# Kernel optimization log

Hardware: AMD Instinct MI355X
Metric: run time of the kernel (lower is better)

Reference implementation:

```python
import jax, jax.numpy as jnp
import numpy as np

NX = 1024
N_HEAD = 16
HEAD_DIM = NX // N_HEAD
RPE_MAX = 20
LN_EPS = 1e-5


def _layernorm(h, g, b, eps=LN_EPS):
    mu = jnp.mean(h, axis=-1, keepdims=True)
    var = jnp.var(h, axis=-1, keepdims=True)
    return (h - mu) * jax.lax.rsqrt(var + eps) * g + b


def setup_inputs() -> dict:
    key = jax.random.key(0)
    ks = jax.random.split(key, 12)
    B, S = 2, 1024
    x = jax.random.normal(ks[0], (B, S, NX), dtype=jnp.float32)
    local_info = jax.random.normal(ks[1], (B, S, NX), dtype=jnp.float32)
    attention_mask = jnp.zeros((B, 1, 1, S), dtype=jnp.float32)
    pairwise_dist = jax.random.randint(ks[2], (B, S, S), -RPE_MAX, RPE_MAX + 1, dtype=jnp.int32)
    s = 0.02
    Wqkv = jax.random.normal(ks[3], (NX, 3 * NX), dtype=jnp.float32) * s
    bqkv = jnp.zeros((3 * NX,), dtype=jnp.float32)
    Wproj = jax.random.normal(ks[4], (NX, NX), dtype=jnp.float32) * s
    bproj = jnp.zeros((NX,), dtype=jnp.float32)
    rpek = jax.random.normal(ks[5], (2 * RPE_MAX + 1, HEAD_DIM), dtype=jnp.float32) * s
    ln1_g = jnp.ones((NX,), dtype=jnp.float32)
    ln1_b = jnp.zeros((NX,), dtype=jnp.float32)
    gate_W = jax.random.normal(ks[6], (2 * NX, NX), dtype=jnp.float32) * s
    return {"x": x, "local_info": local_info, "attention_mask": attention_mask,
            "pairwise_dist": pairwise_dist, "Wqkv": Wqkv, "bqkv": bqkv,
            "Wproj": Wproj, "bproj": bproj, "rpek": rpek,
            "ln1_g": ln1_g, "ln1_b": ln1_b, "gate_W": gate_W}


def reference(x, local_info, attention_mask, pairwise_dist, Wqkv, bqkv, Wproj, bproj, rpek, ln1_g, ln1_b, gate_W):
    B, S, _ = x.shape
    qkv = x @ Wqkv + bqkv                      # [B,S,3*NX]
    q, k, v = jnp.split(qkv, 3, axis=-1)
    q = q.reshape(B, S, N_HEAD, HEAD_DIM)
    k = k.reshape(B, S, N_HEAD, HEAD_DIM)
    v = v.reshape(B, S, N_HEAD, HEAD_DIM)
    # content scores [B,H,Q,K]
    w = jnp.einsum('bqhd,bkhd->bhqk', q, k)
    # relative-position bias: embedding lookup + per-query matmul
    k_rpe = rpek[pairwise_dist + RPE_MAX]      # [B,Q,K,D]
    w_rpe = jnp.einsum('bqhd,bqkd->bhqk', q, k_rpe)
    w = (w + w_rpe) / jnp.float32(HEAD_DIM) ** 0.5
    w = w + attention_mask
    p = jax.nn.softmax(w, axis=-1)
    a = jnp.einsum('bhqk,bkhd->bqhd', p, v).reshape(B, S, NX)
    a = a @ Wproj + bproj
    # residual + LN1
    h = _layernorm(x + a, ln1_g, ln1_b)
    # gated fusion of local and global info
    z = jax.nn.sigmoid(jnp.concatenate([local_info, h], axis=-1) @ gate_W)
    out = (1.0 - z) * h + z * local_info
    return out
```

## Files before the change

### kernel.cpp

```cpp
#include <hip/hip_runtime.h>
#include <hip/hip_bf16.h>

#define SEQ 1024
#define NH 16
#define HD 64
#define NXD 1024

typedef unsigned short u16;
typedef unsigned char u8;
typedef __attribute__((ext_vector_type(8))) short short8;
typedef __attribute__((ext_vector_type(4))) float f32x4;

__device__ __forceinline__ u16 f2bf(float f) {
    __hip_bfloat16 h = __float2bfloat16(f);
    u16 u; __builtin_memcpy(&u, &h, 2); return u;
}
__device__ __forceinline__ float bf2f(u16 u) {
    __hip_bfloat16 h; __builtin_memcpy(&h, &u, 2); return __bfloat162float(h);
}

__device__ __forceinline__ void gld16(const void* g, void* l) {
    __builtin_amdgcn_global_load_lds(
        (const __attribute__((address_space(1))) void*)g,
        (__attribute__((address_space(3))) void*)l, 16, 0, 0);
}

template<int N> __device__ __forceinline__ void waitcnt_vm() {
    asm volatile("s_waitcnt vmcnt(%0)" :: "n"(N) : "memory");
}
__device__ __forceinline__ void raw_barrier() {
    asm volatile("s_barrier" ::: "memory");
}

__device__ __forceinline__ int swz(int row, int k) { return k ^ ((row & 7) << 3); }

__device__ __forceinline__ void transpose_tile(const float* __restrict__ src,
        u16* __restrict__ dst, int R, int C, int bx, int by) {
    __shared__ float tile[32][33];
    int r0 = by * 32, c0 = bx * 32;
    int tr = threadIdx.x >> 3, tc = (threadIdx.x & 7) * 4;
    float4 v = *(const float4*)(src + (size_t)(r0 + tr) * C + c0 + tc);
    tile[tr][tc+0] = v.x; tile[tr][tc+1] = v.y; tile[tr][tc+2] = v.z; tile[tr][tc+3] = v.w;
    __syncthreads();
    int row = c0 + tr;
    int kk  = r0 + tc;
    u16* d = dst + (size_t)row * R + swz(row, kk);
    #pragma unroll
    for (int j = 0; j < 4; j++) d[j] = f2bf(tile[tc+j][tr]);
}

__global__ __launch_bounds__(256) void prep_all(const float* __restrict__ x,
        const float* __restrict__ local, const int* __restrict__ pd,
        const float* __restrict__ Wqkv, const float* __restrict__ Wproj,
        const float* __restrict__ gateW,
        u16* __restrict__ xb, u16* __restrict__ gateA, u8* __restrict__ pdu8,
        u16* __restrict__ WqkvT, u16* __restrict__ WprojT, u16* __restrict__ gateWT) {
    int bid = blockIdx.x;
    if (bid < 2048) {
        int i = (bid * 256 + threadIdx.x) * 4;
        int row = i >> 10, c = i & 1023;
        float4 v = *(const float4*)(x + i);
        u16* d = xb + (size_t)row * 1024 + swz(row, c);
        d[0] = f2bf(v.x); d[1] = f2bf(v.y); d[2] = f2bf(v.z); d[3] = f2bf(v.w);
    } else if (bid < 4096) {
        int i = ((bid - 2048) * 256 + threadIdx.x) * 4;
        int row = i >> 10, c = i & 1023;
        float4 v = *(const float4*)(local + i);
        u16* d = gateA + (size_t)row * 2048 + swz(row, c);
        d[0] = f2bf(v.x); d[1] = f2bf(v.y); d[2] = f2bf(v.z); d[3] = f2bf(v.w);
    } else if (bid < 6144) {
        int i = ((bid - 4096) * 256 + threadIdx.x) * 4;
        int4 v = *(const int4*)(pd + i);
        uchar4 o;
        o.x = (u8)(v.x + 20); o.y = (u8)(v.y + 20);
        o.z = (u8)(v.z + 20); o.w = (u8)(v.w + 20);
        *(uchar4*)(pdu8 + i) = o;
    } else if (bid < 9216) {
        int k = bid - 6144;  transpose_tile(Wqkv,  WqkvT,  1024, 3072, k % 96, k / 96);
    } else if (bid < 10240) {
        int k = bid - 9216;  transpose_tile(Wproj, WprojT, 1024, 1024, k % 32, k / 32);
    } else {
        int k = bid - 10240; transpose_tile(gateW, gateWT, 2048, 1024, k % 32, k / 32);
    }
}

__global__ __launch_bounds__(256) void trq_kernel(const u16* __restrict__ vb,
        u16* __restrict__ vTb, const u16* __restrict__ qb,
        const float* __restrict__ rpek, u16* __restrict__ qrpe16) {
    int bid = blockIdx.x;
    if (bid < 2048) {
        __shared__ u16 tile[32][33];
        int bh = bid >> 6, d0 = ((bid >> 5) & 1) * 32, s0 = (bid & 31) * 32;
        int tr = threadIdx.x >> 3, tc = (threadIdx.x & 7) * 4;
        const u16* s = vb + ((size_t)bh * SEQ + s0 + tr) * HD + d0 + tc;
        #pragma unroll
        for (int j = 0; j < 4; j++) tile[tr][tc+j] = s[j];
        __syncthreads();
        int kt = s0 >> 6, sbase = (s0 & 32) + tc, drow = d0 + tr;
        u16* d = vTb + (((size_t)bh * 16 + kt) * 64 + drow) * 64 + swz(drow, sbase);
        #pragma unroll
        for (int j = 0; j < 4; j++) d[j] = tile[tc+j][tr];
    } else {
        int t = threadIdx.x, lane = t & 63, wid = t >> 6;
        int quad = lane >> 4, l16 = lane & 15;
        int r0 = ((bid - 2048) * 4 + wid) * 16;
        short8 af[2];
        #pragma unroll
        for (int s = 0; s < 2; s++)
            af[s] = *(const short8*)(qb + (size_t)(r0 + l16) * HD + s * 32 + quad * 8);
        #pragma unroll
        for (int nt = 0; nt < 3; nt++) {
            int n = nt * 16 + l16;
            const float* rp = rpek + (size_t)(n < 41 ? n : 40) * HD;
            f32x4 acc = {0.f, 0.f, 0.f, 0.f};
            #pragma unroll
            for (int s = 0; s < 2; s++) {
                float4 f0 = *(const float4*)(rp + s * 32 + quad * 8);
                float4 f1 = *(const float4*)(rp + s * 32 + quad * 8 + 4);
                short8 bf;
                bf[0] = (short)f2bf(f0.x); bf[1] = (short)f2bf(f0.y);
                bf[2] = (short)f2bf(f0.z); bf[3] = (short)f2bf(f0.w);
                bf[4] = (short)f2bf(f1.x); bf[5] = (short)f2bf(f1.y);
                bf[6] = (short)f2bf(f1.z); bf[7] = (short)f2bf(f1.w);
                acc = __builtin_amdgcn_mfma_f32_16x16x32_bf16(af[s], bf, acc, 0, 0, 0);
            }
            if (n < 41) {
                #pragma unroll
                for (int r = 0; r < 4; r++)
                    qrpe16[(size_t)(r0 + quad * 4 + r) * 48 + n] = f2bf(acc[r]);
            }
        }
    }
}

template<int BM, int BN, int EPI, int CHX, int CHY>
__global__ __launch_bounds__(256) void gemm_bt(
        const u16* __restrict__ A, int lda, const u16* __restrict__ BT, int K,
        const float* __restrict__ bias, float* __restrict__ out_f,
        u16* __restrict__ oq, u16* __restrict__ ok, u16* __restrict__ ov,
        const u16* __restrict__ h16, const float* __restrict__ loc32,
        float* __restrict__ outg) {
    const int MT = BM / 32, NT = BN / 32;
    const int LPT = BM / 32 + BN / 32;
    __shared__ u16 Al[2][BM * 64];
    __shared__ u16 Bl[2][BN * 64];
    int t = threadIdx.x, lane = t & 63, wid = t >> 6;
    int quad = lane >> 4, l16 = lane & 15;
    int id = blockIdx.x + (CHX * 4) * blockIdx.y;
    int xcd = id & 7, li = id >> 3;
    int bxs = (xcd & 3) * CHX + li % CHX;
    int bys = (xcd >> 2) * CHY + li / CHX;
    int m0 = bys * BM, n0 = bxs * BN;
    int waveM = wid >> 1, waveN = wid & 1;
    f32x4 acc[MT][NT] = {};

    auto stage = [&](int buf, int k0) {
        #pragma unroll
        for (int i = 0; i < BM / 32; i++) {
            int c = t + i * 256;
            gld16(A + (size_t)(m0 + (c >> 3)) * lda + k0 + (c & 7) * 8,
                  &Al[buf][(c & ~63) * 8]);
        }
        #pragma unroll
        for (int i = 0; i < BN / 32; i++) {
            int c = t + i * 256;
            gld16(BT + (size_t)(n0 + (c >> 3)) * K + k0 + (c & 7) * 8,
                  &Bl[buf][(c & ~63) * 8]);
        }
    };

    const int NTILES = K >> 6;
    stage(0, 0);
    for (int tt = 0; tt < NTILES; tt++) {
        int cur = tt & 1;
        raw_barrier();
        if (tt + 1 < NTILES) {
            stage(cur ^ 1, (tt + 1) << 6);
            waitcnt_vm<LPT>();
        } else {
            waitcnt_vm<0>();
        }
        raw_barrier();
        const u16* Ac = Al[cur];
        const u16* Bc = Bl[cur];
        short8 af[MT][2], bfr[NT][2];
        #pragma unroll
        for (int s = 0; s < 2; s++) {
            int xk = (s * 4 + quad) ^ (l16 & 7);
            #pragma unroll
            for (int mt = 0; mt < MT; mt++)
                af[mt][s] = *(const short8*)&Ac[((waveM * (BM / 2) + mt * 16 + l16) * 8 + xk) * 8];
            #pragma unroll
            for (int nt = 0; nt < NT; nt++)
                bfr[nt][s] = *(const short8*)&Bc[((waveN * (BN / 2) + nt * 16 + l16) * 8 + xk) * 8];
        }
        #pragma unroll
        for (int mt = 0; mt < MT; mt++)
            #pragma unroll
            for (int nt = 0; nt < NT; nt++) {
                acc[mt][nt] = __builtin_amdgcn_mfma_f32_16x16x32_bf16(af[mt][0], bfr[nt][0], acc[mt][nt], 0, 0, 0);
                acc[mt][nt] = __builtin_amdgcn_mfma_f32_16x16x32_bf16(af[mt][1], bfr[nt][1], acc[mt][nt], 0, 0, 0);
            }
    }
    #pragma unroll
    for (int mt = 0; mt < MT; mt++)
        #pragma unroll
        for (int nt = 0; nt < NT; nt++)
            #pragma unroll
            for (int r = 0; r < 4; r++) {
                int row = m0 + waveM * (BM / 2) + mt * 16 + quad * 4 + r;
                int col = n0 + waveN * (BN / 2) + nt * 16 + l16;
                float val = acc[mt][nt][r];
                if (EPI == 0) {
                    val += bias[col];
                    int b = row >> 10, s = row & 1023;
                    int sec = col >> 10, cc = col & 1023;
                    int h = cc >> 6, d = cc & 63;
                    u16 bv = f2bf(val);
                    size_t base = ((size_t)(b * NH + h)) * SEQ + s;
                    if (sec == 0)      oq[base * HD + d] = bv;
                    else if (sec == 1) ok[base * HD + swz(s, d)] = bv;
                    else               ov[base * HD + d] = bv;
                } else if (EPI == 1) {
                    out_f[(size_t)row * 1024 + col] = val + bias[col];
                } else {
                    float z = 1.f / (1.f + __expf(-val));
                    size_t idx = (size_t)row * 1024 + col;
                    float hv = bf2f(h16[(size_t)row * 2048 + 1024 + swz(row, col)]);
                    outg[idx] = (1.f - z) * hv + z * loc32[idx];
                }
            }
}

__global__ __launch_bounds__(256) void attn_kernel(
        const u16* __restrict__ qb, const u16* __restrict__ kmat,
        const u16* __restrict__ vTb, const u16* __restrict__ qrpe16,
        const u8* __restrict__ pdu8, const float* __restrict__ mask,
        u16* __restrict__ po0, u16* __restrict__ po1, float* __restrict__ pl) {
    __shared__ u16 Kl[64 * 64];
    __shared__ u16 Vl[64 * 64];
    __shared__ u16 Pl[4][8 * 16 * 8];
    __shared__ u16 qr_lds[64 * 48];
    __shared__ u8 pdl[64 * 80];
    int t = threadIdx.x, lane = t & 63, wid = t >> 6;
    int quad = lane >> 4, l16 = lane & 15;

    int id = blockIdx.x;
    int xcd = id & 7, j = id >> 3;
    int b = xcd >> 2;
    int head = ((xcd & 3) << 2) | (j >> 5);
    int qblk = ((j >> 1) & 15) << 6;
    int sp = j & 1;
    int bh = (b << 4) | head;
    int q0 = qblk + wid * 16;

    {
        const u16* src = qrpe16 + ((size_t)bh * SEQ + qblk) * 48;
        { int c = t, c0 = c & ~63; gld16(src + (size_t)c * 8, &qr_lds[c0 * 8]); }
        if (wid < 2) { int c = 256 + t, c0 = c & ~63; gld16(src + (size_t)c * 8, &qr_lds[c0 * 8]); }
    }

    short8 aq[2];
    #pragma unroll
    for (int s = 0; s < 2; s++)
        aq[s] = *(const short8*)(qb + ((size_t)bh * SEQ + q0 + l16) * HD + s * 32 + quad * 8);
    f32x4 o[4] = {};
    float lrow[4] = {0.f, 0.f, 0.f, 0.f};
    u16* Pw = Pl[wid];
    const u8* pdbase = pdu8 + ((size_t)b * SEQ + qblk) * SEQ;
    for (int kt = 0; kt < 8; kt++) {
        int k0 = sp * 512 + kt * 64;
        const u16* kbase = kmat + ((size_t)bh * SEQ + k0) * HD;
        const u16* vbase = vTb + (((size_t)bh * 16 + (k0 >> 6)) * 64) * 64;
        __syncthreads();
        #pragma unroll
        for (int i = 0; i < 2; i++) {
            int c = t + i * 256;
            gld16(kbase + (size_t)c * 8, &Kl[(c & ~63) * 8]);
            gld16(vbase + (size_t)c * 8, &Vl[(c & ~63) * 8]);
        }
        {
            int qrow = t >> 2, kj = (t & 3) * 16;
            uint4 pv = *(const uint4*)(pdbase + (size_t)qrow * SEQ + k0 + kj);
            *(uint4*)&pdl[qrow * 80 + kj] = pv;
        }
        __syncthreads();
        #pragma unroll
        for (int ks = 0; ks < 4; ks++) {
            f32x4 a = {0.f, 0.f, 0.f, 0.f};
            #pragma unroll
            for (int dh = 0; dh < 2; dh++) {
                short8 bk = *(short8*)&Kl[((ks * 16 + l16) * 8 + ((dh * 4 + quad) ^ (l16 & 7))) * 8];
                a = __builtin_amdgcn_mfma_f32_16x16x32_bf16(aq[dh], bk, a, 0, 0, 0);
            }
            int kcol = k0 + ks * 16 + l16;
            float mk = mask[b * SEQ + kcol];
            int kcl = ks * 16 + l16;
            #pragma unroll
            for (int r = 0; r < 4; r++) {
                int ql = wid * 16 + quad * 4 + r;
                int pdv = pdl[ql * 80 + kcl];
                float rpe = bf2f(qr_lds[ql * 48 + pdv]);
                float sc = (a[r] + rpe) * 0.125f + mk;
                float p = __expf(fminf(sc, 30.f));
                lrow[r] += p;
                Pw[((kcl >> 3) * 16 + quad * 4 + r) * 8 + (kcl & 7)] = f2bf(p);
            }
        }
        asm volatile("s_waitcnt lgkmcnt(0)" ::: "memory");
        #pragma unroll
        for (int ks2 = 0; ks2 < 2; ks2++) {
            short8 pa = *(short8*)&Pw[((ks2 * 4 + quad) * 16 + l16) * 8];
            #pragma unroll
            for (int dt = 0; dt < 4; dt++) {
                short8 vv = *(short8*)&Vl[((dt * 16 + l16) * 8 + ((ks2 * 4 + quad) ^ (l16 & 7))) * 8];
                o[dt] = __builtin_amdgcn_mfma_f32_16x16x32_bf16(pa, vv, o[dt], 0, 0, 0);
            }
        }
    }
    #pragma unroll
    for (int r = 0; r < 4; r++) {
        #pragma unroll
        for (int off = 1; off < 16; off <<= 1)
            lrow[r] += __shfl_xor(lrow[r], off, 16);
    }
    u16* po = sp ? po1 : po0;
    #pragma unroll
    for (int r = 0; r < 4; r++) {
        int row = bh * SEQ + q0 + quad * 4 + r;
        #pragma unroll
        for (int dt = 0; dt < 4; dt++)
            po[(size_t)row * 64 + dt * 16 + l16] = f2bf(o[dt][r]);
        if (l16 == 0)
            pl[sp * 32768 + row] = lrow[r];
    }
}

__global__ __launch_bounds__(256) void attn_combine(const u16* __restrict__ po0,
        const u16* __restrict__ po1, const float* __restrict__ pl,
        u16* __restrict__ aoutb) {
    int idx = blockIdx.x * 256 + threadIdx.x;
    int row = idx >> 6, d = idx & 63;
    float l0 = pl[row], l1 = pl[32768 + row];
    float inv = 1.f / (l0 + l1);
    float o0 = bf2f(po0[(size_t)row * 64 + d]);
    float o1 = bf2f(po1[(size_t)row * 64 + d]);
    float val = (o0 + o1) * inv;
    int bh = row >> 10, qrow = row & 1023;
    int b = bh >> 4, h = bh & 15;
    int arow = b * SEQ + qrow;
    aoutb[(size_t)arow * NXD + swz(arow, h * HD + d)] = f2bf(val);
}

__device__ __forceinline__ float block_sum(float v, float* sred) {
    #pragma unroll
    for (int o = 32; o > 0; o >>= 1) v += __shfl_down(v, o, 64);
    int lane = threadIdx.x & 63, wid = threadIdx.x >> 6;
    __syncthreads();
    if (lane == 0) sred[wid] = v;
    __syncthreads();
    return sred[0] + sred[1] + sred[2] + sred[3];
}

__global__ __launch_bounds__(256) void ln_kernel(const float* __restrict__ x,
        const float* __restrict__ a, const float* __restrict__ g,
        const float* __restrict__ bln, u16* __restrict__ gateA) {
    int row = blockIdx.x;
    __shared__ float sred[4];
    float vals[4];
    float s = 0.f;
    #pragma unroll
    for (int i = 0; i < 4; i++) {
        int c = threadIdx.x + i * 256;
        vals[i] = x[(size_t)row * NXD + c] + a[(size_t)row * NXD + c];
        s += vals[i];
    }
    s = block_sum(s, sred);
    float mu = s * (1.f / NXD);
    float vs = 0.f;
    #pragma unroll
    for (int i = 0; i < 4; i++) { float d = vals[i] - mu; vs += d * d; }
    vs = block_sum(vs, sred);
    float rstd = rsqrtf(vs * (1.f / NXD) + 1e-5f);
    #pragma unroll
    for (int i = 0; i < 4; i++) {
        int c = threadIdx.x + i * 256;
        float hv = (vals[i] - mu) * rstd * g[c] + bln[c];
        gateA[(size_t)row * 2048 + 1024 + swz(row, c)] = f2bf(hv);
    }
}

extern "C" void kernel_launch(void* const* d_in, const int* in_sizes, int n_in,
                              void* d_out, int out_size, void* d_ws, size_t ws_size,
                              hipStream_t stream) {
    const float* x     = (const float*)d_in[0];
    const float* local = (const float*)d_in[1];
    const float* mask  = (const float*)d_in[2];
    const int*   pd    = (const int*)d_in[3];
    const float* Wqkv  = (const float*)d_in[4];
    const float* bqkv  = (const float*)d_in[5];
    const float* Wproj = (const float*)d_in[6];
    const float* bproj = (const float*)d_in[7];
    const float* rpek  = (const float*)d_in[8];
    const float* ln_g  = (const float*)d_in[9];
    const float* ln_b  = (const float*)d_in[10];
    const float* gateW = (const float*)d_in[11];
    float* out = (float*)d_out;

    char* ws = (char*)d_ws;
    const size_t MB = 1u << 20;
    u16*   xb    = (u16*)(ws + 0);
    u16*   WqkvT = (u16*)(ws + 4 * MB);
    u16*   po0   = (u16*)(ws + 4 * MB);
    float* pl    = (float*)(ws + 8 * MB);
    u16*   WprojT= (u16*)(ws + 10 * MB);
    u16*   qb    = (u16*)(ws + 12 * MB);
    u16*   kb    = (u16*)(ws + 16 * MB);
    u16*   vb    = (u16*)(ws + 20 * MB);
    u16*   po1   = (u16*)(ws + 20 * MB);
    float* pout  = (float*)(ws + 16 * MB);
    u16*   vTb   = (u16*)(ws + 24 * MB);
    u16*   qrpe16= (u16*)(ws + 28 * MB);
    u16*   gateA = (u16*)(ws + 34 * MB);
    u8*    pdu8  = (u8*)(ws + 42 * MB);
    u16*   gateWT= (u16*)(ws + 44 * MB);
    u16*   aoutb = xb;

    prep_all<<<12288, 256, 0, stream>>>(x, local, pd, Wqkv, Wproj, gateW,
            xb, gateA, pdu8, WqkvT, WprojT, gateWT);
    gemm_bt<128, 64, 0, 12, 8><<<dim3(48, 16), 256, 0, stream>>>(xb, 1024, WqkvT, 1024, bqkv,
            nullptr, qb, kb, vb, nullptr, nullptr, nullptr);
    trq_kernel<<<2560, 256, 0, stream>>>(vb, vTb, qb, rpek, qrpe16);
    attn_kernel<<<1024, 256, 0, stream>>>(qb, kb, vTb, qrpe16, pdu8, mask,
            po0, po1, pl);
    attn_combine<<<8192, 256, 0, stream>>>(po0, po1, pl, aoutb);
    gemm_bt<64, 64, 1, 4, 16><<<dim3(16, 32), 256, 0, stream>>>(aoutb, 1024, WprojT, 1024, bproj,
            pout, nullptr, nullptr, nullptr, nullptr, nullptr, nullptr);
    ln_kernel<<<2048, 256, 0, stream>>>(x, pout, ln_g, ln_b, gateA);
    gemm_bt<64, 64, 2, 4, 16><<<dim3(16, 32), 256, 0, stream>>>(gateA, 2048, gateWT, 2048, nullptr,
            nullptr, nullptr, nullptr, nullptr, gateA, local, out);
}
```

Baseline: 217.5 us.

## Fuse V transpose, q·rpe, and split-K combine into QKV GEMM and attention

The QKV GEMM epilogue now writes V straight into the transposed, swizzled tile layout, which removes the separate transpose pass. The q·rpek projection moves into the attention kernel's prologue and is written to LDS rather than a global buffer. The two-way key split and its combine kernel are dropped: each block now walks all 16 key tiles and normalizes its output directly. This saves two launches and several global round trips, but halves the attention grid to 512 blocks and doubles the serial loop per block, so parallelism drops.

```diff
diff --git a/kernel.cpp b/kernel.cpp
--- a/kernel.cpp
+++ b/kernel.cpp
@@ -84,55 +84,6 @@
     }
 }
 
-__global__ __launch_bounds__(256) void trq_kernel(const u16* __restrict__ vb,
-        u16* __restrict__ vTb, const u16* __restrict__ qb,
-        const float* __restrict__ rpek, u16* __restrict__ qrpe16) {
-    int bid = blockIdx.x;
-    if (bid < 2048) {
-        __shared__ u16 tile[32][33];
-        int bh = bid >> 6, d0 = ((bid >> 5) & 1) * 32, s0 = (bid & 31) * 32;
-        int tr = threadIdx.x >> 3, tc = (threadIdx.x & 7) * 4;
-        const u16* s = vb + ((size_t)bh * SEQ + s0 + tr) * HD + d0 + tc;
-        #pragma unroll
-        for (int j = 0; j < 4; j++) tile[tr][tc+j] = s[j];
-        __syncthreads();
-        int kt = s0 >> 6, sbase = (s0 & 32) + tc, drow = d0 + tr;
-        u16* d = vTb + (((size_t)bh * 16 + kt) * 64 + drow) * 64 + swz(drow, sbase);
-        #pragma unroll
-        for (int j = 0; j < 4; j++) d[j] = tile[tc+j][tr];
-    } else {
-        int t = threadIdx.x, lane = t & 63, wid = t >> 6;
-        int quad = lane >> 4, l16 = lane & 15;
-        int r0 = ((bid - 2048) * 4 + wid) * 16;
-        short8 af[2];
-        #pragma unroll
-        for (int s = 0; s < 2; s++)
-            af[s] = *(const short8*)(qb + (size_t)(r0 + l16) * HD + s * 32 + quad * 8);
-        #pragma unroll
-        for (int nt = 0; nt < 3; nt++) {
-            int n = nt * 16 + l16;
-            const float* rp = rpek + (size_t)(n < 41 ? n : 40) * HD;
-            f32x4 acc = {0.f, 0.f, 0.f, 0.f};
-            #pragma unroll
-            for (int s = 0; s < 2; s++) {
-                float4 f0 = *(const float4*)(rp + s * 32 + quad * 8);
-                float4 f1 = *(const float4*)(rp + s * 32 + quad * 8 + 4);
-                short8 bf;
-                bf[0] = (short)f2bf(f0.x); bf[1] = (short)f2bf(f0.y);
-                bf[2] = (short)f2bf(f0.z); bf[3] = (short)f2bf(f0.w);
-                bf[4] = (short)f2bf(f1.x); bf[5] = (short)f2bf(f1.y);
-                bf[6] = (short)f2bf(f1.z); bf[7] = (short)f2bf(f1.w);
-                acc = __builtin_amdgcn_mfma_f32_16x16x32_bf16(af[s], bf, acc, 0, 0, 0);
-            }
-            if (n < 41) {
-                #pragma unroll
-                for (int r = 0; r < 4; r++)
-                    qrpe16[(size_t)(r0 + quad * 4 + r) * 48 + n] = f2bf(acc[r]);
-            }
-        }
-    }
-}
-
 template<int BM, int BN, int EPI, int CHX, int CHY>
 __global__ __launch_bounds__(256) void gemm_bt(
         const u16* __restrict__ A, int lda, const u16* __restrict__ BT, int K,
@@ -217,10 +168,10 @@
                     int sec = col >> 10, cc = col & 1023;
                     int h = cc >> 6, d = cc & 63;
                     u16 bv = f2bf(val);
-                    size_t base = ((size_t)(b * NH + h)) * SEQ + s;
-                    if (sec == 0)      oq[base * HD + d] = bv;
-                    else if (sec == 1) ok[base * HD + swz(s, d)] = bv;
-                    else               ov[base * HD + d] = bv;
+                    size_t bh = (size_t)(b * NH + h);
+                    if (sec == 0)      oq[(bh * SEQ + s) * HD + d] = bv;
+                    else if (sec == 1) ok[(bh * SEQ + s) * HD + swz(s, d)] = bv;
+                    else               ov[((bh * 16 + (s >> 6)) * 64 + d) * 64 + swz(d, s & 63)] = bv;
                 } else if (EPI == 1) {
                     out_f[(size_t)row * 1024 + col] = val + bias[col];
                 } else {
@@ -234,9 +185,9 @@
 
 __global__ __launch_bounds__(256) void attn_kernel(
         const u16* __restrict__ qb, const u16* __restrict__ kmat,
-        const u16* __restrict__ vTb, const u16* __restrict__ qrpe16,
+        const u16* __restrict__ vTb, const float* __restrict__ rpek,
         const u8* __restrict__ pdu8, const float* __restrict__ mask,
-        u16* __restrict__ po0, u16* __restrict__ po1, float* __restrict__ pl) {
+        u16* __restrict__ aoutb) {
     __shared__ u16 Kl[64 * 64];
     __shared__ u16 Vl[64 * 64];
     __shared__ u16 Pl[4][8 * 16 * 8];
@@ -248,30 +199,47 @@
     int id = blockIdx.x;
     int xcd = id & 7, j = id >> 3;
     int b = xcd >> 2;
-    int head = ((xcd & 3) << 2) | (j >> 5);
-    int qblk = ((j >> 1) & 15) << 6;
-    int sp = j & 1;
+    int head = ((xcd & 3) << 2) | (j >> 4);
+    int qblk = (j & 15) << 6;
     int bh = (b << 4) | head;
     int q0 = qblk + wid * 16;
 
-    {
-        const u16* src = qrpe16 + ((size_t)bh * SEQ + qblk) * 48;
-        { int c = t, c0 = c & ~63; gld16(src + (size_t)c * 8, &qr_lds[c0 * 8]); }
-        if (wid < 2) { int c = 256 + t, c0 = c & ~63; gld16(src + (size_t)c * 8, &qr_lds[c0 * 8]); }
-    }
-
     short8 aq[2];
     #pragma unroll
     for (int s = 0; s < 2; s++)
         aq[s] = *(const short8*)(qb + ((size_t)bh * SEQ + q0 + l16) * HD + s * 32 + quad * 8);
+
+    #pragma unroll
+    for (int nt = 0; nt < 3; nt++) {
+        int n = nt * 16 + l16;
+        const float* rp = rpek + (size_t)(n < 41 ? n : 40) * HD;
+        f32x4 acc = {0.f, 0.f, 0.f, 0.f};
+        #pragma unroll
+        for (int s = 0; s < 2; s++) {
+            float4 f0 = *(const float4*)(rp + s * 32 + quad * 8);
+            float4 f1 = *(const float4*)(rp + s * 32 + quad * 8 + 4);
+            short8 bf;
+            bf[0] = (short)f2bf(f0.x); bf[1] = (short)f2bf(f0.y);
+            bf[2] = (short)f2bf(f0.z); bf[3] = (short)f2bf(f0.w);
+            bf[4] = (short)f2bf(f1.x); bf[5] = (short)f2bf(f1.y);
+            bf[6] = (short)f2bf(f1.z); bf[7] = (short)f2bf(f1.w);
+            acc = __builtin_amdgcn_mfma_f32_16x16x32_bf16(aq[s], bf, acc, 0, 0, 0);
+        }
+        if (n < 41) {
+            #pragma unroll
+            for (int r = 0; r < 4; r++)
+                qr_lds[(wid * 16 + quad * 4 + r) * 48 + n] = f2bf(acc[r]);
+        }
+    }
+
     f32x4 o[4] = {};
     float lrow[4] = {0.f, 0.f, 0.f, 0.f};
     u16* Pw = Pl[wid];
     const u8* pdbase = pdu8 + ((size_t)b * SEQ + qblk) * SEQ;
-    for (int kt = 0; kt < 8; kt++) {
-        int k0 = sp * 512 + kt * 64;
+    for (int kt = 0; kt < 16; kt++) {
+        int k0 = kt * 64;
         const u16* kbase = kmat + ((size_t)bh * SEQ + k0) * HD;
-        const u16* vbase = vTb + (((size_t)bh * 16 + (k0 >> 6)) * 64) * 64;
+        const u16* vbase = vTb + (((size_t)bh * 16 + kt) * 64) * 64;
         __syncthreads();
         #pragma unroll
         for (int i = 0; i < 2; i++) {
@@ -324,32 +292,16 @@
         for (int off = 1; off < 16; off <<= 1)
             lrow[r] += __shfl_xor(lrow[r], off, 16);
     }
-    u16* po = sp ? po1 : po0;
     #pragma unroll
     for (int r = 0; r < 4; r++) {
-        int row = bh * SEQ + q0 + quad * 4 + r;
-        #pragma unroll
-        for (int dt = 0; dt < 4; dt++)
-            po[(size_t)row * 64 + dt * 16 + l16] = f2bf(o[dt][r]);
-        if (l16 == 0)
-            pl[sp * 32768 + row] = lrow[r];
-    }
-}
-
-__global__ __launch_bounds__(256) void attn_combine(const u16* __restrict__ po0,
-        const u16* __restrict__ po1, const float* __restrict__ pl,
-        u16* __restrict__ aoutb) {
-    int idx = blockIdx.x * 256 + threadIdx.x;
-    int row = idx >> 6, d = idx & 63;
-    float l0 = pl[row], l1 = pl[32768 + row];
-    float inv = 1.f / (l0 + l1);
-    float o0 = bf2f(po0[(size_t)row * 64 + d]);
-    float o1 = bf2f(po1[(size_t)row * 64 + d]);
-    float val = (o0 + o1) * inv;
-    int bh = row >> 10, qrow = row & 1023;
-    int b = bh >> 4, h = bh & 15;
-    int arow = b * SEQ + qrow;
-    aoutb[(size_t)arow * NXD + swz(arow, h * HD + d)] = f2bf(val);
+        int arow = b * SEQ + q0 + quad * 4 + r;
+        float inv = 1.f / lrow[r];
+        #pragma unroll
+        for (int dt = 0; dt < 4; dt++) {
+            int col = head * HD + dt * 16 + l16;
+            aoutb[(size_t)arow * NXD + swz(arow, col)] = f2bf(o[dt][r] * inv);
+        }
+    }
 }
 
 __device__ __forceinline__ float block_sum(float v, float* sred) {
@@ -411,16 +363,11 @@
     const size_t MB = 1u << 20;
     u16*   xb    = (u16*)(ws + 0);
     u16*   WqkvT = (u16*)(ws + 4 * MB);
-    u16*   po0   = (u16*)(ws + 4 * MB);
-    float* pl    = (float*)(ws + 8 * MB);
     u16*   WprojT= (u16*)(ws + 10 * MB);
     u16*   qb    = (u16*)(ws + 12 * MB);
     u16*   kb    = (u16*)(ws + 16 * MB);
-    u16*   vb    = (u16*)(ws + 20 * MB);
-    u16*   po1   = (u16*)(ws + 20 * MB);
     float* pout  = (float*)(ws + 16 * MB);
     u16*   vTb   = (u16*)(ws + 24 * MB);
-    u16*   qrpe16= (u16*)(ws + 28 * MB);
     u16*   gateA = (u16*)(ws + 34 * MB);
     u8*    pdu8  = (u8*)(ws + 42 * MB);
     u16*   gateWT= (u16*)(ws + 44 * MB);
@@ -429,11 +376,8 @@
     prep_all<<<12288, 256, 0, stream>>>(x, local, pd, Wqkv, Wproj, gateW,
             xb, gateA, pdu8, WqkvT, WprojT, gateWT);
     gemm_bt<128, 64, 0, 12, 8><<<dim3(48, 16), 256, 0, stream>>>(xb, 1024, WqkvT, 1024, bqkv,
-            nullptr, qb, kb, vb, nullptr, nullptr, nullptr);
-    trq_kernel<<<2560, 256, 0, stream>>>(vb, vTb, qb, rpek, qrpe16);
-    attn_kernel<<<1024, 256, 0, stream>>>(qb, kb, vTb, qrpe16, pdu8, mask,
-            po0, po1, pl);
-    attn_combine<<<8192, 256, 0, stream>>>(po0, po1, pl, aoutb);
+            nullptr, qb, kb, vTb, nullptr, nullptr, nullptr);
+    attn_kernel<<<512, 256, 0, stream>>>(qb, kb, vTb, rpek, pdu8, mask, aoutb);
     gemm_bt<64, 64, 1, 4, 16><<<dim3(16, 32), 256, 0, stream>>>(aoutb, 1024, WprojT, 1024, bproj,
             pout, nullptr, nullptr, nullptr, nullptr, nullptr, nullptr);
     ln_kernel<<<2048, 256, 0, stream>>>(x, pout, ln_g, ln_b, gateA);
```

Result: slower. 223.8 us (+2.9%).
